# Kernel tuning notes

Measured on AMD Instinct MI355X. Metric: run time of the kernel, lower is better.

Reference implementation:

```python
import jax, jax.numpy as jnp
import numpy as np

H = 200          # LSTM hidden size
POOL = 16        # maxout pool size


def lstm_step(x, h, c, Wih, Whh, bih, bhh):
    # PyTorch LSTM gate order: i, f, g, o
    gates = x @ Wih.T + h @ Whh.T + bih + bhh  # [4H]
    i, f, g, o = jnp.split(gates, 4)
    i, f, o = jax.nn.sigmoid(i), jax.nn.sigmoid(f), jax.nn.sigmoid(o)
    g = jnp.tanh(g)
    c_new = f * c + i * g
    h_new = o * jnp.tanh(c_new)
    return h_new, c_new


def hmn(U, h, s, e, w1, w2, b2, w3, b3, w4, b4):
    T = U.shape[0]
    r = jnp.tanh(jnp.concatenate([h, s, e]) @ w1.T)                 # [200]
    x = jnp.concatenate([U, jnp.broadcast_to(r, (T, H))], axis=1)    # [T,600]
    m1 = jnp.max((x @ w2.T + b2).reshape(T, POOL, H), axis=1)        # [T,200]
    m2 = jnp.max((m1 @ w3.T + b3).reshape(T, POOL, H), axis=1)       # [T,200]
    a = jnp.max((jnp.concatenate([m1, m2], axis=1) @ w4.T + b4).reshape(T, POOL, 1), axis=1)
    return a[:, 0]                                                   # [T]


def decoder_fwd(U, lstm_Wih, lstm_Whh, lstm_bih, lstm_bhh,
                s_fc1w, s_fc2w, s_fc2b, s_fc3w, s_fc3b, s_fc4w, s_fc4b,
                e_fc1w, e_fc2w, e_fc2b, e_fc3w, e_fc3b, e_fc4w, e_fc4b):
    sp = (s_fc1w, s_fc2w, s_fc2b, s_fc3w, s_fc3b, s_fc4w, s_fc4b)
    ep = (e_fc1w, e_fc2w, e_fc2b, e_fc3w, e_fc3b, e_fc4w, e_fc4b)
    h = jnp.zeros(H, U.dtype)
    c = jnp.zeros(H, U.dtype)
    start = jnp.array(0)
    end = jnp.array(0)

    # iteration 0
    x = jnp.concatenate([U[start], U[end]])
    h, c = lstm_step(x, h, c, lstm_Wih, lstm_Whh, lstm_bih, lstm_bhh)
    alpha = hmn(U, h, U[start], U[end], *sp)
    beta = hmn(U, h, U[start], U[end], *ep)
    start, end = jnp.argmax(alpha), jnp.argmax(beta)
    alphas, betas = [alpha], [beta]
    done = jnp.array(False)

    # iterations 1..3 with early-exit freeze (original breaks when start/end converge)
    for _ in range(3):
        x = jnp.concatenate([U[start], U[end]])
        ch, cc = lstm_step(x, h, c, lstm_Wih, lstm_Whh, lstm_bih, lstm_bhh)
        ca = hmn(U, ch, U[start], U[end], *sp)
        cb = hmn(U, ch, U[start], U[end], *ep)
        ns, ne = jnp.argmax(ca), jnp.argmax(cb)
        alphas.append(jnp.where(done, alphas[-1], ca))
        betas.append(jnp.where(done, betas[-1], cb))
        new_done = done | ((ns == start) & (ne == end))
        h = jnp.where(done, h, ch)
        c = jnp.where(done, c, cc)
        start = jnp.where(done, start, ns)
        end = jnp.where(done, end, ne)
        done = new_done

    return jnp.stack(alphas), jnp.stack(betas)  # each [4, T]


def setup_inputs() -> dict:
    key = jax.random.key(0)
    ks = jax.random.split(key, 24)
    sc = 0.02
    T = 16384
    inp = {
        "U": jax.random.normal(ks[0], (T, 400), dtype=jnp.float32),
        "lstm_Wih": jax.random.normal(ks[1], (4 * H, 800), dtype=jnp.float32) * sc,
        "lstm_Whh": jax.random.normal(ks[2], (4 * H, H), dtype=jnp.float32) * sc,
        "lstm_bih": jnp.zeros(4 * H, jnp.float32),
        "lstm_bhh": jnp.zeros(4 * H, jnp.float32),
    }
    i = 3
    for pre in ("s", "e"):
        inp[pre + "_fc1w"] = jax.random.normal(ks[i], (H, 1000), dtype=jnp.float32) * sc; i += 1
        inp[pre + "_fc2w"] = jax.random.normal(ks[i], (POOL * H, 600), dtype=jnp.float32) * sc; i += 1
        inp[pre + "_fc2b"] = jax.random.normal(ks[i], (POOL * H,), dtype=jnp.float32) * sc; i += 1
        inp[pre + "_fc3w"] = jax.random.normal(ks[i], (POOL * H, H), dtype=jnp.float32) * sc; i += 1
        inp[pre + "_fc3b"] = jax.random.normal(ks[i], (POOL * H,), dtype=jnp.float32) * sc; i += 1
        inp[pre + "_fc4w"] = jax.random.normal(ks[i], (POOL, 2 * H), dtype=jnp.float32) * sc; i += 1
        inp[pre + "_fc4b"] = jax.random.normal(ks[i], (POOL,), dtype=jnp.float32) * sc; i += 1
    return inp


def reference(U, lstm_Wih, lstm_Whh, lstm_bih, lstm_bhh,
              s_fc1w, s_fc2w, s_fc2b, s_fc3w, s_fc3b, s_fc4w, s_fc4b,
              e_fc1w, e_fc2w, e_fc2b, e_fc3w, e_fc3b, e_fc4w, e_fc4b):
    return decoder_fwd(U, lstm_Wih, lstm_Whh, lstm_bih, lstm_bhh,
                       s_fc1w, s_fc2w, s_fc2b, s_fc3w, s_fc3b, s_fc4w, s_fc4b,
                       e_fc1w, e_fc2w, e_fc2b, e_fc3w, e_fc3b, e_fc4w, e_fc4b)
```

## Files before the change

kernel.cpp:

```cpp
#include <hip/hip_runtime.h>
#include <math.h>

#define T_LEN 16384
#define HDIM 200
#define NPOOL 16

typedef __bf16 v8bf __attribute__((ext_vector_type(8)));
typedef float v4f __attribute__((ext_vector_type(4)));

__device__ float g_ca[T_LEN];
__device__ float g_cb[T_LEN];
__device__ float g_rw2s[NPOOL * HDIM];
__device__ float g_rw2e[NPOOL * HDIM];
__device__ float g_gates[4 * HDIM];
__device__ float g_h[HDIM];
__device__ float g_c[HDIM];
__device__ float g_ch[HDIM];
__device__ float g_cc[HDIM];
__device__ float g_rs[HDIM];
__device__ float g_re[HDIM];
__device__ int   g_ctrl[17];
__device__ __align__(16) unsigned short g_Ubf[T_LEN * 400];
__device__ __align__(16) unsigned short g_w2bf[2][3200 * 416];
__device__ __align__(16) unsigned short g_w3bf[2][3200 * 224];
__device__ __align__(16) unsigned short g_w4a[2][16 * 448];
__device__ __align__(16) unsigned short g_m1[2][T_LEN * 224];
__device__ __align__(16) unsigned short g_m2[2][T_LEN * 224];

__device__ inline unsigned short f2bf(float f) {
    unsigned int u = __builtin_bit_cast(unsigned int, f);
    unsigned int r = u + 0x7FFFu + ((u >> 16) & 1u);
    return (unsigned short)(r >> 16);
}
__device__ inline v8bf zero8() {
    return __builtin_bit_cast(v8bf, make_uint4(0u, 0u, 0u, 0u));
}
__device__ inline int clampT(int v) {
    return v < 0 ? 0 : (v >= T_LEN ? T_LEN - 1 : v);
}

__device__ inline void gl_lds16(const unsigned short* g, unsigned short* l) {
    __builtin_amdgcn_global_load_lds(
        (const __attribute__((address_space(1))) unsigned int*)g,
        (__attribute__((address_space(3))) unsigned int*)l,
        16, 0, 0);
}

#define CU_CH   819200
#define C2_CH   166400
#define C3_CH   89600
#define W4A_CH  1792
#define PZ_CH   196608
#define TOT_CH  (CU_CH + 2*C2_CH + 2*C3_CH + W4A_CH + PZ_CH)

__device__ inline void cvt_chunk(const float* __restrict__ src, unsigned short* __restrict__ dst,
                                 int src_stride, int cpr, int ncc, int idx) {
    int r = idx / cpr, c = idx - r * cpr;
    unsigned short o[8] = {0, 0, 0, 0, 0, 0, 0, 0};
    if (c < ncc) {
        const float* s = src + r * src_stride + c * 8;
        float4 f0 = reinterpret_cast<const float4*>(s)[0];
        float4 f1 = reinterpret_cast<const float4*>(s)[1];
        o[0] = f2bf(f0.x); o[1] = f2bf(f0.y); o[2] = f2bf(f0.z); o[3] = f2bf(f0.w);
        o[4] = f2bf(f1.x); o[5] = f2bf(f1.y); o[6] = f2bf(f1.z); o[7] = f2bf(f1.w);
    }
    *reinterpret_cast<uint4*>(dst + r * (cpr * 8) + c * 8) = *reinterpret_cast<uint4*>(o);
}

__global__ void k_cvt_all(const float* __restrict__ U,
                          const float* __restrict__ s_w2, const float* __restrict__ e_w2,
                          const float* __restrict__ s_w3, const float* __restrict__ e_w3,
                          const float* __restrict__ s_w4, const float* __restrict__ e_w4) {
    int i = blockIdx.x * 256 + threadIdx.x;
    if (i < CU_CH) { cvt_chunk(U, g_Ubf, 400, 50, 50, i); return; }
    i -= CU_CH;
    if (i < C2_CH) { cvt_chunk(s_w2, g_w2bf[0], 600, 52, 50, i); return; }
    i -= C2_CH;
    if (i < C2_CH) { cvt_chunk(e_w2, g_w2bf[1], 600, 52, 50, i); return; }
    i -= C2_CH;
    if (i < C3_CH) { cvt_chunk(s_w3, g_w3bf[0], 200, 28, 25, i); return; }
    i -= C3_CH;
    if (i < C3_CH) { cvt_chunk(e_w3, g_w3bf[1], 200, 28, 25, i); return; }
    i -= C3_CH;
    if (i < W4A_CH) {
        int net = i / 896, rem = i - net * 896;
        int r = rem / 56, c = rem - r * 56;
        const float* src = net ? e_w4 : s_w4;
        unsigned short o[8];
#pragma unroll
        for (int j = 0; j < 8; j++) {
            int k = c * 8 + j;
            float v = 0.f;
            if (k < 200) v = src[r * 400 + k];
            else if (k >= 224 && k < 424) v = src[r * 400 + (k - 24)];
            o[j] = f2bf(v);
        }
        *reinterpret_cast<uint4*>(&g_w4a[net][r * 448 + c * 8]) = *reinterpret_cast<uint4*>(o);
        return;
    }
    i -= W4A_CH;
    if (i < PZ_CH) {
        int buf = i / 98304, rem = i - buf * 98304;
        int net = rem / 49152, rem2 = rem - net * 49152;
        int row = rem2 / 3, c = rem2 - row * 3;
        unsigned short* dst = (buf ? g_m2[net] : g_m1[net]) + row * 224 + 200 + c * 8;
        *reinterpret_cast<uint4*>(dst) = make_uint4(0u, 0u, 0u, 0u);
        return;
    }
    i -= PZ_CH;
    if (i < HDIM) { g_h[i] = 0.f; g_c[i] = 0.f; return; }
    i -= HDIM;
    if (i == 0) { g_ctrl[0] = 0; g_ctrl[1] = 0; g_ctrl[2] = 0; }
}

__global__ void k_gates(const float* __restrict__ U,
                        const float* __restrict__ Wih,
                        const float* __restrict__ Whh,
                        const float* __restrict__ bih,
                        const float* __restrict__ bhh,
                        int k) {
    int row = blockIdx.x * 16 + (threadIdx.x >> 4);
    int l = threadIdx.x & 15;
    int start = clampT(g_ctrl[k * 3 + 0]), end = clampT(g_ctrl[k * 3 + 1]);
    float sum = 0.f;
    for (int j = l; j < 800; j += 16) {
        float xv = (j < 400) ? U[start * 400 + j] : U[end * 400 + (j - 400)];
        sum += Wih[row * 800 + j] * xv;
    }
    for (int j = l; j < HDIM; j += 16)
        sum += Whh[row * HDIM + j] * g_h[j];
    for (int off = 8; off > 0; off >>= 1) sum += __shfl_xor(sum, off, 16);
    if (l == 0) g_gates[row] = sum + bih[row] + bhh[row];
}

__global__ void k_r(const float* __restrict__ U,
                    const float* __restrict__ s_w1,
                    const float* __restrict__ e_w1,
                    int k) {
    __shared__ float ch_s[HDIM];
    int t = threadIdx.x;
    if (t < HDIM) {
        float gi = g_gates[t], gf = g_gates[HDIM + t];
        float gg = g_gates[2 * HDIM + t], go = g_gates[3 * HDIM + t];
        float si = 1.f / (1.f + expf(-gi));
        float sf = 1.f / (1.f + expf(-gf));
        float so = 1.f / (1.f + expf(-go));
        float tg = tanhf(gg);
        float cn = sf * g_c[t] + si * tg;
        float hv = so * tanhf(cn);
        ch_s[t] = hv;
        if (blockIdx.x == 0) { g_ch[t] = hv; g_cc[t] = cn; }
    }
    __syncthreads();
    int g = blockIdx.x * 16 + (threadIdx.x >> 4);
    int l = threadIdx.x & 15;
    int net = g / HDIM, i = g % HDIM;
    const float* w1 = net ? e_w1 : s_w1;
    int start = clampT(g_ctrl[k * 3 + 0]), end = clampT(g_ctrl[k * 3 + 1]);
    float sum = 0.f;
    for (int j = l; j < 1000; j += 16) {
        float cv;
        if (j < 200) cv = ch_s[j];
        else if (j < 600) cv = U[start * 400 + (j - 200)];
        else cv = U[end * 400 + (j - 600)];
        sum += w1[i * 1000 + j] * cv;
    }
    for (int off = 8; off > 0; off >>= 1) sum += __shfl_xor(sum, off, 16);
    if (l == 0) { float* out = net ? g_re : g_rs; out[i] = tanhf(sum); }
}

__global__ void k_rw2(const float* __restrict__ s_w2,
                      const float* __restrict__ s_b2,
                      const float* __restrict__ e_w2,
                      const float* __restrict__ e_b2) {
    int g = blockIdx.x * 16 + (threadIdx.x >> 4);
    int l = threadIdx.x & 15;
    int net = g / 3200, n = g % 3200;
    const float* w2 = net ? e_w2 : s_w2;
    const float* b2 = net ? e_b2 : s_b2;
    const float* r = net ? g_re : g_rs;
    float sum = 0.f;
    for (int j = l; j < HDIM; j += 16)
        sum += w2[n * 600 + 400 + j] * r[j];
    for (int off = 8; off > 0; off >>= 1) sum += __shfl_xor(sum, off, 16);
    if (l == 0) { float* out = net ? g_rw2e : g_rw2s; out[n] = sum + b2[n]; }
}

__global__ __launch_bounds__(128, 2) void k_m1() {
    const int bid = blockIdx.x;
    const int net = (bid >> 2) & 1;
    const int r = (bid >> 3) * 4 + (bid & 3);
    const int third = r % 3;
    const int m0 = (r / 3) * 64;
    const unsigned short* w2 = g_w2bf[net];
    const float* rw2 = net ? g_rw2e : g_rw2s;
    unsigned short* m1o = g_m1[net];
    __shared__ __align__(16) unsigned short Bs[2][6656];
    const int tid = threadIdx.x;
    const int lane = tid & 63, wave = tid >> 6;
    const int q = lane >> 4, col = lane & 15, qo = q * 8;
    const int rowb = m0 + wave * 32;
    const int njt = (third == 0) ? 5 : 4;
    const int T2 = njt * 16;

    v8bf a1[2][13];
#pragma unroll
    for (int s = 0; s < 2; s++) {
        const unsigned short* ap = g_Ubf + (rowb + s * 16 + col) * 400 + qo;
#pragma unroll
        for (int ks = 0; ks < 13; ks++) {
            if (ks < 12 || q < 2) a1[s][ks] = *reinterpret_cast<const v8bf*>(ap + ks * 32);
            else a1[s][ks] = zero8();
        }
    }
    {
        const unsigned short* gb = w2 + (third * 16 + col) * 416 + qo;
        for (int c = wave; c < 13; c += 2) gl_lds16(gb + c * 32, &Bs[0][c * 512]);
    }
    v4f mx0, mx1;
    for (int t = 0; t < T2; t++) {
        __syncthreads();
        if (t + 1 < T2) {
            int jtn = ((t + 1) >> 4) * 3 + third, pn = (t + 1) & 15;
            int j0n = (jtn < 12) ? jtn * 16 : 184;
            const unsigned short* gb = w2 + (pn * HDIM + j0n + col) * 416 + qo;
            unsigned short* lb = Bs[(t + 1) & 1];
            for (int c = wave; c < 13; c += 2) gl_lds16(gb + c * 32, lb + c * 512);
        }
        const unsigned short* bb = Bs[t & 1];
        int jt = (t >> 4) * 3 + third, p = t & 15;
        int j0 = (jt < 12) ? jt * 16 : 184;
        int n = j0 + col;
        if (p == 0) {
            mx0 = (v4f){-INFINITY, -INFINITY, -INFINITY, -INFINITY};
            mx1 = mx0;
        }
        v4f a00 = {0.f, 0.f, 0.f, 0.f}, a01 = a00, a10 = a00, a11 = a00;
#pragma unroll
        for (int ks = 0; ks < 12; ks += 2) {
            v8bf b0 = *reinterpret_cast<const v8bf*>(&bb[ks * 512 + lane * 8]);
            a00 = __builtin_amdgcn_mfma_f32_16x16x32_bf16(a1[0][ks], b0, a00, 0, 0, 0);
            a10 = __builtin_amdgcn_mfma_f32_16x16x32_bf16(a1[1][ks], b0, a10, 0, 0, 0);
            v8bf b1 = *reinterpret_cast<const v8bf*>(&bb[(ks + 1) * 512 + lane * 8]);
            a01 = __builtin_amdgcn_mfma_f32_16x16x32_bf16(a1[0][ks + 1], b1, a01, 0, 0, 0);
            a11 = __builtin_amdgcn_mfma_f32_16x16x32_bf16(a1[1][ks + 1], b1, a11, 0, 0, 0);
        }
        {
            v8bf b0 = *reinterpret_cast<const v8bf*>(&bb[12 * 512 + lane * 8]);
            a00 = __builtin_amdgcn_mfma_f32_16x16x32_bf16(a1[0][12], b0, a00, 0, 0, 0);
            a10 = __builtin_amdgcn_mfma_f32_16x16x32_bf16(a1[1][12], b0, a10, 0, 0, 0);
        }
        float rv = rw2[p * HDIM + n];
#pragma unroll
        for (int i = 0; i < 4; i++) {
            mx0[i] = fmaxf(mx0[i], a00[i] + a01[i] + rv);
            mx1[i] = fmaxf(mx1[i], a10[i] + a11[i] + rv);
        }
        if (p == 15) {
#pragma unroll
            for (int i = 0; i < 4; i++) {
                m1o[(rowb + q * 4 + i) * 224 + n] = f2bf(mx0[i]);
                m1o[(rowb + 16 + q * 4 + i) * 224 + n] = f2bf(mx1[i]);
            }
        }
    }
}

__global__ __launch_bounds__(128, 2) void k_m2(
    const float* __restrict__ b3s, const float* __restrict__ b3e) {
    const int bid = blockIdx.x;
    const int net = (bid >> 2) & 1;
    const int r = (bid >> 3) * 4 + (bid & 3);
    const int third = r % 3;
    const int m0 = (r / 3) * 64;
    const unsigned short* w3 = g_w3bf[net];
    const float* b3 = net ? b3e : b3s;
    unsigned short* m2o = g_m2[net];
    __shared__ __align__(16) unsigned short Bs[2][3584];
    const int tid = threadIdx.x;
    const int lane = tid & 63, wave = tid >> 6;
    const int q = lane >> 4, col = lane & 15, qo = q * 8;
    const int rowb = m0 + wave * 32;
    const int njt = (third == 0) ? 5 : 4;
    const int T2 = njt * 16;

    v8bf a2[2][7];
#pragma unroll
    for (int s = 0; s < 2; s++) {
        const unsigned short* ap = g_m1[net] + (rowb + s * 16 + col) * 224 + qo;
#pragma unroll
        for (int ks = 0; ks < 7; ks++)
            a2[s][ks] = *reinterpret_cast<const v8bf*>(ap + ks * 32);
    }
    {
        const unsigned short* gb = w3 + (third * 16 + col) * 224 + qo;
        for (int c = wave; c < 7; c += 2) gl_lds16(gb + c * 32, &Bs[0][c * 512]);
    }
    v4f mx0, mx1;
    for (int t = 0; t < T2; t++) {
        __syncthreads();
        if (t + 1 < T2) {
            int jtn = ((t + 1) >> 4) * 3 + third, pn = (t + 1) & 15;
            int j0n = (jtn < 12) ? jtn * 16 : 184;
            const unsigned short* gb = w3 + (pn * HDIM + j0n + col) * 224 + qo;
            unsigned short* lb = Bs[(t + 1) & 1];
            for (int c = wave; c < 7; c += 2) gl_lds16(gb + c * 32, lb + c * 512);
        }
        const unsigned short* bb = Bs[t & 1];
        int jt = (t >> 4) * 3 + third, p = t & 15;
        int j0 = (jt < 12) ? jt * 16 : 184;
        int n = j0 + col;
        if (p == 0) {
            mx0 = (v4f){-INFINITY, -INFINITY, -INFINITY, -INFINITY};
            mx1 = mx0;
        }
        v4f a00 = {0.f, 0.f, 0.f, 0.f}, a01 = a00, a10 = a00, a11 = a00;
#pragma unroll
        for (int ks = 0; ks < 6; ks += 2) {
            v8bf b0 = *reinterpret_cast<const v8bf*>(&bb[ks * 512 + lane * 8]);
            a00 = __builtin_amdgcn_mfma_f32_16x16x32_bf16(a2[0][ks], b0, a00, 0, 0, 0);
            a10 = __builtin_amdgcn_mfma_f32_16x16x32_bf16(a2[1][ks], b0, a10, 0, 0, 0);
            v8bf b1 = *reinterpret_cast<const v8bf*>(&bb[(ks + 1) * 512 + lane * 8]);
            a01 = __builtin_amdgcn_mfma_f32_16x16x32_bf16(a2[0][ks + 1], b1, a01, 0, 0, 0);
            a11 = __builtin_amdgcn_mfma_f32_16x16x32_bf16(a2[1][ks + 1], b1, a11, 0, 0, 0);
        }
        {
            v8bf b0 = *reinterpret_cast<const v8bf*>(&bb[6 * 512 + lane * 8]);
            a00 = __builtin_amdgcn_mfma_f32_16x16x32_bf16(a2[0][6], b0, a00, 0, 0, 0);
            a10 = __builtin_amdgcn_mfma_f32_16x16x32_bf16(a2[1][6], b0, a10, 0, 0, 0);
        }
        float bv = b3[p * HDIM + n];
#pragma unroll
        for (int i = 0; i < 4; i++) {
            mx0[i] = fmaxf(mx0[i], a00[i] + a01[i] + bv);
            mx1[i] = fmaxf(mx1[i], a10[i] + a11[i] + bv);
        }
        if (p == 15) {
#pragma unroll
            for (int i = 0; i < 4; i++) {
                m2o[(rowb + q * 4 + i) * 224 + n] = f2bf(mx0[i]);
                m2o[(rowb + 16 + q * 4 + i) * 224 + n] = f2bf(mx1[i]);
            }
        }
    }
}

__global__ __launch_bounds__(128) void k_alpha(
    const float* __restrict__ b4s, const float* __restrict__ b4e) {
    const int bid = blockIdx.x;
    const int net = (bid >> 2) & 1;
    const int m0 = ((bid >> 3) * 4 + (bid & 3)) * 64;
    const unsigned short* w4 = g_w4a[net];
    const float* b4 = net ? b4e : b4s;
    float* outv = net ? g_cb : g_ca;
    const int tid = threadIdx.x;
    const int lane = tid & 63, wave = tid >> 6;
    const int q = lane >> 4, col = lane & 15, qo = q * 8;
    const int rowb = m0 + wave * 32;

    v4f ac0 = {0.f, 0.f, 0.f, 0.f}, ac1 = ac0;
#pragma unroll
    for (int half = 0; half < 2; half++) {
        const unsigned short* src = half ? g_m2[net] : g_m1[net];
#pragma unroll
        for (int ks = 0; ks < 7; ks++) {
            v8bf b = *reinterpret_cast<const v8bf*>(&w4[col * 448 + half * 224 + ks * 32 + qo]);
            v8bf x0 = *reinterpret_cast<const v8bf*>(src + (rowb + col) * 224 + ks * 32 + qo);
            ac0 = __builtin_amdgcn_mfma_f32_16x16x32_bf16(x0, b, ac0, 0, 0, 0);
            v8bf x1 = *reinterpret_cast<const v8bf*>(src + (rowb + 16 + col) * 224 + ks * 32 + qo);
            ac1 = __builtin_amdgcn_mfma_f32_16x16x32_bf16(x1, b, ac1, 0, 0, 0);
        }
    }
    float bbi = b4[col];
#pragma unroll
    for (int s = 0; s < 2; s++) {
        v4f ac = s ? ac1 : ac0;
        float v0 = ac[0] + bbi, v1 = ac[1] + bbi, v2 = ac[2] + bbi, v3 = ac[3] + bbi;
        for (int off = 1; off < 16; off <<= 1) {
            v0 = fmaxf(v0, __shfl_xor(v0, off, 16));
            v1 = fmaxf(v1, __shfl_xor(v1, off, 16));
            v2 = fmaxf(v2, __shfl_xor(v2, off, 16));
            v3 = fmaxf(v3, __shfl_xor(v3, off, 16));
        }
        if (col == 0) {
            const int tb = rowb + s * 16 + q * 4;
            outv[tb + 0] = v0;
            outv[tb + 1] = v1;
            outv[tb + 2] = v2;
            outv[tb + 3] = v3;
        }
    }
}

__global__ void k_commit(int k, float* __restrict__ out) {
    int done = g_ctrl[k * 3 + 2];
    if (blockIdx.x < 128) {
        int is_beta = blockIdx.x >= 64;
        int t = ((int)blockIdx.x & 63) * 256 + threadIdx.x;
        float* row = out + (is_beta ? 4 * T_LEN : 0) + k * T_LEN;
        if (done) row[t] = row[t - T_LEN];
        else row[t] = (is_beta ? g_cb : g_ca)[t];
    } else {
        __shared__ float sv[256];
        __shared__ int si[256];
        int ns = 0, ne = 0;
        for (int which = 0; which < 2; which++) {
            const float* src = which ? g_cb : g_ca;
            float best = -INFINITY;
            int bi = T_LEN - 1;
            for (int t = threadIdx.x; t < T_LEN; t += 256) {
                float v = src[t];
                if (v > best) { best = v; bi = t; }
            }
            sv[threadIdx.x] = best; si[threadIdx.x] = bi;
            __syncthreads();
            for (int s = 128; s > 0; s >>= 1) {
                if (threadIdx.x < s) {
                    float ov = sv[threadIdx.x + s]; int oi = si[threadIdx.x + s];
                    if (ov > sv[threadIdx.x] || (ov == sv[threadIdx.x] && oi < si[threadIdx.x])) {
                        sv[threadIdx.x] = ov; si[threadIdx.x] = oi;
                    }
                }
                __syncthreads();
            }
            if (which == 0) ns = clampT(si[0]); else ne = clampT(si[0]);
            __syncthreads();
        }
        int t = threadIdx.x;
        if (t < HDIM && !done) { g_h[t] = g_ch[t]; g_c[t] = g_cc[t]; }
        if (t == 0) {
            int sp = g_ctrl[k * 3 + 0], ep = g_ctrl[k * 3 + 1];
            if (done) {
                g_ctrl[(k + 1) * 3 + 0] = sp;
                g_ctrl[(k + 1) * 3 + 1] = ep;
                g_ctrl[(k + 1) * 3 + 2] = 1;
            } else {
                g_ctrl[(k + 1) * 3 + 0] = ns;
                g_ctrl[(k + 1) * 3 + 1] = ne;
                g_ctrl[(k + 1) * 3 + 2] = (k == 0) ? 0 : ((ns == sp && ne == ep) ? 1 : 0);
            }
        }
    }
}

extern "C" void kernel_launch(void* const* d_in, const int* in_sizes, int n_in,
                              void* d_out, int out_size, void* d_ws, size_t ws_size,
                              hipStream_t stream) {
    const float* U    = (const float*)d_in[0];
    const float* Wih  = (const float*)d_in[1];
    const float* Whh  = (const float*)d_in[2];
    const float* bih  = (const float*)d_in[3];
    const float* bhh  = (const float*)d_in[4];
    const float* s_w1 = (const float*)d_in[5];
    const float* s_w2 = (const float*)d_in[6];
    const float* s_b2 = (const float*)d_in[7];
    const float* s_w3 = (const float*)d_in[8];
    const float* s_b3 = (const float*)d_in[9];
    const float* s_w4 = (const float*)d_in[10];
    const float* s_b4 = (const float*)d_in[11];
    const float* e_w1 = (const float*)d_in[12];
    const float* e_w2 = (const float*)d_in[13];
    const float* e_b2 = (const float*)d_in[14];
    const float* e_w3 = (const float*)d_in[15];
    const float* e_b3 = (const float*)d_in[16];
    const float* e_w4 = (const float*)d_in[17];
    const float* e_b4 = (const float*)d_in[18];
    float* out = (float*)d_out;
    (void)d_ws; (void)ws_size; (void)in_sizes; (void)n_in; (void)out_size;

    const int cvt_blocks = (TOT_CH + HDIM + 1 + 255) / 256;
    k_cvt_all<<<cvt_blocks, 256, 0, stream>>>(U, s_w2, e_w2, s_w3, e_w3, s_w4, e_w4);

    for (int k = 0; k < 4; k++) {
        k_gates<<<50, 256, 0, stream>>>(U, Wih, Whh, bih, bhh, k);
        k_r<<<25, 256, 0, stream>>>(U, s_w1, e_w1, k);
        k_rw2<<<400, 256, 0, stream>>>(s_w2, s_b2, e_w2, e_b2);
        k_m1<<<1536, 128, 0, stream>>>();
        k_m2<<<1536, 128, 0, stream>>>(s_b3, e_b3);
        k_alpha<<<512, 128, 0, stream>>>(s_b4, e_b4);
        k_commit<<<129, 256, 0, stream>>>(k, out);
    }
}
```

Measured before the change: 1.255 ms.

## Load maxout weights directly to registers and double rows per block

The m1 and m2 maxout GEMM kernels drop the LDS double-buffered weight staging and its per-step barriers. Each wave now loads its weight fragments straight from global memory into registers. Blocks grow from 2 to 4 waves, covering 128 rows each, and launch with half as many blocks. This removes LDS traffic and syncs, but each wave now fetches the weights separately, so global and L2 traffic goes up and per-thread register pressure rises.

Measured after the change: 1.608 ms. 1.28x slower.

```diff
diff --git a/kernel.cpp b/kernel.cpp
--- a/kernel.cpp
+++ b/kernel.cpp
@@ -37,13 +37,6 @@
 }
 __device__ inline int clampT(int v) {
     return v < 0 ? 0 : (v >= T_LEN ? T_LEN - 1 : v);
-}
-
-__device__ inline void gl_lds16(const unsigned short* g, unsigned short* l) {
-    __builtin_amdgcn_global_load_lds(
-        (const __attribute__((address_space(1))) unsigned int*)g,
-        (__attribute__((address_space(3))) unsigned int*)l,
-        16, 0, 0);
 }
 
 #define CU_CH   819200
@@ -186,22 +179,20 @@
     if (l == 0) { float* out = net ? g_rw2e : g_rw2s; out[n] = sum + b2[n]; }
 }
 
-__global__ __launch_bounds__(128, 2) void k_m1() {
+__global__ __launch_bounds__(256, 2) void k_m1() {
     const int bid = blockIdx.x;
     const int net = (bid >> 2) & 1;
     const int r = (bid >> 3) * 4 + (bid & 3);
     const int third = r % 3;
-    const int m0 = (r / 3) * 64;
+    const int m0 = (r / 3) * 128;
     const unsigned short* w2 = g_w2bf[net];
     const float* rw2 = net ? g_rw2e : g_rw2s;
     unsigned short* m1o = g_m1[net];
-    __shared__ __align__(16) unsigned short Bs[2][6656];
     const int tid = threadIdx.x;
     const int lane = tid & 63, wave = tid >> 6;
     const int q = lane >> 4, col = lane & 15, qo = q * 8;
     const int rowb = m0 + wave * 32;
     const int njt = (third == 0) ? 5 : 4;
-    const int T2 = njt * 16;
 
     v8bf a1[2][13];
 #pragma unroll
@@ -213,76 +204,61 @@
             else a1[s][ks] = zero8();
         }
     }
-    {
-        const unsigned short* gb = w2 + (third * 16 + col) * 416 + qo;
-        for (int c = wave; c < 13; c += 2) gl_lds16(gb + c * 32, &Bs[0][c * 512]);
-    }
-    v4f mx0, mx1;
-    for (int t = 0; t < T2; t++) {
-        __syncthreads();
-        if (t + 1 < T2) {
-            int jtn = ((t + 1) >> 4) * 3 + third, pn = (t + 1) & 15;
-            int j0n = (jtn < 12) ? jtn * 16 : 184;
-            const unsigned short* gb = w2 + (pn * HDIM + j0n + col) * 416 + qo;
-            unsigned short* lb = Bs[(t + 1) & 1];
-            for (int c = wave; c < 13; c += 2) gl_lds16(gb + c * 32, lb + c * 512);
-        }
-        const unsigned short* bb = Bs[t & 1];
-        int jt = (t >> 4) * 3 + third, p = t & 15;
-        int j0 = (jt < 12) ? jt * 16 : 184;
-        int n = j0 + col;
-        if (p == 0) {
-            mx0 = (v4f){-INFINITY, -INFINITY, -INFINITY, -INFINITY};
-            mx1 = mx0;
-        }
-        v4f a00 = {0.f, 0.f, 0.f, 0.f}, a01 = a00, a10 = a00, a11 = a00;
-#pragma unroll
-        for (int ks = 0; ks < 12; ks += 2) {
-            v8bf b0 = *reinterpret_cast<const v8bf*>(&bb[ks * 512 + lane * 8]);
-            a00 = __builtin_amdgcn_mfma_f32_16x16x32_bf16(a1[0][ks], b0, a00, 0, 0, 0);
-            a10 = __builtin_amdgcn_mfma_f32_16x16x32_bf16(a1[1][ks], b0, a10, 0, 0, 0);
-            v8bf b1 = *reinterpret_cast<const v8bf*>(&bb[(ks + 1) * 512 + lane * 8]);
-            a01 = __builtin_amdgcn_mfma_f32_16x16x32_bf16(a1[0][ks + 1], b1, a01, 0, 0, 0);
-            a11 = __builtin_amdgcn_mfma_f32_16x16x32_bf16(a1[1][ks + 1], b1, a11, 0, 0, 0);
-        }
-        {
-            v8bf b0 = *reinterpret_cast<const v8bf*>(&bb[12 * 512 + lane * 8]);
-            a00 = __builtin_amdgcn_mfma_f32_16x16x32_bf16(a1[0][12], b0, a00, 0, 0, 0);
-            a10 = __builtin_amdgcn_mfma_f32_16x16x32_bf16(a1[1][12], b0, a10, 0, 0, 0);
-        }
-        float rv = rw2[p * HDIM + n];
+
+    for (int jc = 0; jc < njt; jc++) {
+        const int jt = jc * 3 + third;
+        const int j0 = (jt < 12) ? jt * 16 : 184;
+        const int n = j0 + col;
+        const unsigned short* wb = w2 + n * 416 + qo;
+        v4f mx0 = {-INFINITY, -INFINITY, -INFINITY, -INFINITY};
+        v4f mx1 = mx0;
+#pragma unroll 1
+        for (int p = 0; p < NPOOL; p++) {
+            const unsigned short* bp = wb + p * (HDIM * 416);
+            v8bf b[13];
+#pragma unroll
+            for (int ks = 0; ks < 13; ks++)
+                b[ks] = *reinterpret_cast<const v8bf*>(bp + ks * 32);
+            v4f a00 = {0.f, 0.f, 0.f, 0.f}, a01 = a00, a10 = a00, a11 = a00;
+#pragma unroll
+            for (int ks = 0; ks < 12; ks += 2) {
+                a00 = __builtin_amdgcn_mfma_f32_16x16x32_bf16(a1[0][ks], b[ks], a00, 0, 0, 0);
+                a10 = __builtin_amdgcn_mfma_f32_16x16x32_bf16(a1[1][ks], b[ks], a10, 0, 0, 0);
+                a01 = __builtin_amdgcn_mfma_f32_16x16x32_bf16(a1[0][ks + 1], b[ks + 1], a01, 0, 0, 0);
+                a11 = __builtin_amdgcn_mfma_f32_16x16x32_bf16(a1[1][ks + 1], b[ks + 1], a11, 0, 0, 0);
+            }
+            a00 = __builtin_amdgcn_mfma_f32_16x16x32_bf16(a1[0][12], b[12], a00, 0, 0, 0);
+            a10 = __builtin_amdgcn_mfma_f32_16x16x32_bf16(a1[1][12], b[12], a10, 0, 0, 0);
+            float rv = rw2[p * HDIM + n];
+#pragma unroll
+            for (int i = 0; i < 4; i++) {
+                mx0[i] = fmaxf(mx0[i], a00[i] + a01[i] + rv);
+                mx1[i] = fmaxf(mx1[i], a10[i] + a11[i] + rv);
+            }
+        }
 #pragma unroll
         for (int i = 0; i < 4; i++) {
-            mx0[i] = fmaxf(mx0[i], a00[i] + a01[i] + rv);
-            mx1[i] = fmaxf(mx1[i], a10[i] + a11[i] + rv);
-        }
-        if (p == 15) {
-#pragma unroll
-            for (int i = 0; i < 4; i++) {
-                m1o[(rowb + q * 4 + i) * 224 + n] = f2bf(mx0[i]);
-                m1o[(rowb + 16 + q * 4 + i) * 224 + n] = f2bf(mx1[i]);
-            }
-        }
-    }
-}
-
-__global__ __launch_bounds__(128, 2) void k_m2(
+            m1o[(rowb + q * 4 + i) * 224 + n] = f2bf(mx0[i]);
+            m1o[(rowb + 16 + q * 4 + i) * 224 + n] = f2bf(mx1[i]);
+        }
+    }
+}
+
+__global__ __launch_bounds__(256, 2) void k_m2(
     const float* __restrict__ b3s, const float* __restrict__ b3e) {
     const int bid = blockIdx.x;
     const int net = (bid >> 2) & 1;
     const int r = (bid >> 3) * 4 + (bid & 3);
     const int third = r % 3;
-    const int m0 = (r / 3) * 64;
+    const int m0 = (r / 3) * 128;
     const unsigned short* w3 = g_w3bf[net];
     const float* b3 = net ? b3e : b3s;
     unsigned short* m2o = g_m2[net];
-    __shared__ __align__(16) unsigned short Bs[2][3584];
     const int tid = threadIdx.x;
     const int lane = tid & 63, wave = tid >> 6;
     const int q = lane >> 4, col = lane & 15, qo = q * 8;
     const int rowb = m0 + wave * 32;
     const int njt = (third == 0) ? 5 : 4;
-    const int T2 = njt * 16;
 
     v8bf a2[2][7];
 #pragma unroll
@@ -292,55 +268,42 @@
         for (int ks = 0; ks < 7; ks++)
             a2[s][ks] = *reinterpret_cast<const v8bf*>(ap + ks * 32);
     }
-    {
-        const unsigned short* gb = w3 + (third * 16 + col) * 224 + qo;
-        for (int c = wave; c < 7; c += 2) gl_lds16(gb + c * 32, &Bs[0][c * 512]);
-    }
-    v4f mx0, mx1;
-    for (int t = 0; t < T2; t++) {
-        __syncthreads();
-        if (t + 1 < T2) {
-            int jtn = ((t + 1) >> 4) * 3 + third, pn = (t + 1) & 15;
-            int j0n = (jtn < 12) ? jtn * 16 : 184;
-            const unsigned short* gb = w3 + (pn * HDIM + j0n + col) * 224 + qo;
-            unsigned short* lb = Bs[(t + 1) & 1];
-            for (int c = wave; c < 7; c += 2) gl_lds16(gb + c * 32, lb + c * 512);
-        }
-        const unsigned short* bb = Bs[t & 1];
-        int jt = (t >> 4) * 3 + third, p = t & 15;
-        int j0 = (jt < 12) ? jt * 16 : 184;
-        int n = j0 + col;
-        if (p == 0) {
-            mx0 = (v4f){-INFINITY, -INFINITY, -INFINITY, -INFINITY};
-            mx1 = mx0;
-        }
-        v4f a00 = {0.f, 0.f, 0.f, 0.f}, a01 = a00, a10 = a00, a11 = a00;
-#pragma unroll
-        for (int ks = 0; ks < 6; ks += 2) {
-            v8bf b0 = *reinterpret_cast<const v8bf*>(&bb[ks * 512 + lane * 8]);
-            a00 = __builtin_amdgcn_mfma_f32_16x16x32_bf16(a2[0][ks], b0, a00, 0, 0, 0);
-            a10 = __builtin_amdgcn_mfma_f32_16x16x32_bf16(a2[1][ks], b0, a10, 0, 0, 0);
-            v8bf b1 = *reinterpret_cast<const v8bf*>(&bb[(ks + 1) * 512 + lane * 8]);
-            a01 = __builtin_amdgcn_mfma_f32_16x16x32_bf16(a2[0][ks + 1], b1, a01, 0, 0, 0);
-            a11 = __builtin_amdgcn_mfma_f32_16x16x32_bf16(a2[1][ks + 1], b1, a11, 0, 0, 0);
-        }
-        {
-            v8bf b0 = *reinterpret_cast<const v8bf*>(&bb[6 * 512 + lane * 8]);
-            a00 = __builtin_amdgcn_mfma_f32_16x16x32_bf16(a2[0][6], b0, a00, 0, 0, 0);
-            a10 = __builtin_amdgcn_mfma_f32_16x16x32_bf16(a2[1][6], b0, a10, 0, 0, 0);
-        }
-        float bv = b3[p * HDIM + n];
+
+    for (int jc = 0; jc < njt; jc++) {
+        const int jt = jc * 3 + third;
+        const int j0 = (jt < 12) ? jt * 16 : 184;
+        const int n = j0 + col;
+        const unsigned short* wb = w3 + n * 224 + qo;
+        v4f mx0 = {-INFINITY, -INFINITY, -INFINITY, -INFINITY};
+        v4f mx1 = mx0;
+#pragma unroll 1
+        for (int p = 0; p < NPOOL; p++) {
+            const unsigned short* bp = wb + p * (HDIM * 224);
+            v8bf b[7];
+#pragma unroll
+            for (int ks = 0; ks < 7; ks++)
+                b[ks] = *reinterpret_cast<const v8bf*>(bp + ks * 32);
+            v4f a00 = {0.f, 0.f, 0.f, 0.f}, a01 = a00, a10 = a00, a11 = a00;
+#pragma unroll
+            for (int ks = 0; ks < 6; ks += 2) {
+                a00 = __builtin_amdgcn_mfma_f32_16x16x32_bf16(a2[0][ks], b[ks], a00, 0, 0, 0);
+                a10 = __builtin_amdgcn_mfma_f32_16x16x32_bf16(a2[1][ks], b[ks], a10, 0, 0, 0);
+                a01 = __builtin_amdgcn_mfma_f32_16x16x32_bf16(a2[0][ks + 1], b[ks + 1], a01, 0, 0, 0);
+                a11 = __builtin_amdgcn_mfma_f32_16x16x32_bf16(a2[1][ks + 1], b[ks + 1], a11, 0, 0, 0);
+            }
+            a00 = __builtin_amdgcn_mfma_f32_16x16x32_bf16(a2[0][6], b[6], a00, 0, 0, 0);
+            a10 = __builtin_amdgcn_mfma_f32_16x16x32_bf16(a2[1][6], b[6], a10, 0, 0, 0);
+            float bv = b3[p * HDIM + n];
+#pragma unroll
+            for (int i = 0; i < 4; i++) {
+                mx0[i] = fmaxf(mx0[i], a00[i] + a01[i] + bv);
+                mx1[i] = fmaxf(mx1[i], a10[i] + a11[i] + bv);
+            }
+        }
 #pragma unroll
         for (int i = 0; i < 4; i++) {
-            mx0[i] = fmaxf(mx0[i], a00[i] + a01[i] + bv);
-            mx1[i] = fmaxf(mx1[i], a10[i] + a11[i] + bv);
-        }
-        if (p == 15) {
-#pragma unroll
-            for (int i = 0; i < 4; i++) {
-                m2o[(rowb + q * 4 + i) * 224 + n] = f2bf(mx0[i]);
-                m2o[(rowb + 16 + q * 4 + i) * 224 + n] = f2bf(mx1[i]);
-            }
+            m2o[(rowb + q * 4 + i) * 224 + n] = f2bf(mx0[i]);
+            m2o[(rowb + 16 + q * 4 + i) * 224 + n] = f2bf(mx1[i]);
         }
     }
 }
@@ -475,8 +438,8 @@
         k_gates<<<50, 256, 0, stream>>>(U, Wih, Whh, bih, bhh, k);
         k_r<<<25, 256, 0, stream>>>(U, s_w1, e_w1, k);
         k_rw2<<<400, 256, 0, stream>>>(s_w2, s_b2, e_w2, e_b2);
-        k_m1<<<1536, 128, 0, stream>>>();
-        k_m2<<<1536, 128, 0, stream>>>(s_b3, e_b3);
+        k_m1<<<768, 256, 0, stream>>>();
+        k_m2<<<768, 256, 0, stream>>>(s_b3, e_b3);
         k_alpha<<<512, 128, 0, stream>>>(s_b4, e_b4);
         k_commit<<<129, 256, 0, stream>>>(k, out);
     }
```
